# Kernel tuning notes

Hardware: AMD Instinct MI355X
Metric: run time of the kernel (lower is better)

The kernel has to match this reference:

```python
import jax, jax.numpy as jnp
import numpy as np
from jax.scipy.linalg import expm

B, S, D, E, K, NROT = 2, 2048, 1024, 8, 2, 3
EPS = 1e-5


def setup_inputs() -> dict:
    key = jax.random.key(0)
    ks = jax.random.split(key, 16)
    sc = 0.02
    x = jax.random.normal(ks[0], (B, S, D), jnp.float32)
    ln_gamma = 1.0 + sc * jax.random.normal(ks[1], (D,), jnp.float32)
    ln_beta = sc * jax.random.normal(ks[2], (D,), jnp.float32)
    abel_w = sc * jax.random.normal(ks[3], (D, D), jnp.float32)
    abel_b = sc * jax.random.normal(ks[4], (D,), jnp.float32)
    moe_gate_w = sc * jax.random.normal(ks[5], (D, E), jnp.float32)
    moe_gate_b = sc * jax.random.normal(ks[6], (E,), jnp.float32)
    ew1 = sc * jax.random.normal(ks[7], (E, D, 2 * D), jnp.float32)
    eb1 = sc * jax.random.normal(ks[8], (E, 2 * D), jnp.float32)
    ew2 = sc * jax.random.normal(ks[9], (E, 2 * D, D), jnp.float32)
    eb2 = sc * jax.random.normal(ks[10], (E, D), jnp.float32)
    g = sc * jax.random.normal(ks[11], (NROT, D, D), jnp.float32)
    gens = 0.5 * (g - jnp.swapaxes(g, -1, -2))  # skew-symmetric, as in reset_parameters
    gc_w = sc * jax.random.normal(ks[12], (2 * D, 1), jnp.float32)
    gc_b = sc * jax.random.normal(ks[13], (1,), jnp.float32)
    return dict(x=x, ln_gamma=ln_gamma, ln_beta=ln_beta, abel_w=abel_w, abel_b=abel_b,
                moe_gate_w=moe_gate_w, moe_gate_b=moe_gate_b, ew1=ew1, eb1=eb1,
                ew2=ew2, eb2=eb2, gens=gens, gc_w=gc_w, gc_b=gc_b)


def _gelu(x):
    return jax.nn.gelu(x, approximate=False)  # torch nn.GELU default = exact erf


def _forward(x, ln_gamma, ln_beta, abel_w, abel_b, moe_gate_w, moe_gate_b,
             ew1, eb1, ew2, eb2, gens, gc_w, gc_b):
    residual = x
    # LayerNorm
    mu = jnp.mean(x, axis=-1, keepdims=True)
    var = jnp.mean((x - mu) ** 2, axis=-1, keepdims=True)
    xn = (x - mu) * jax.lax.rsqrt(var + EPS) * ln_gamma + ln_beta
    # abel branch: Linear + GELU
    abel_out = _gelu(xn @ abel_w + abel_b)
    # MoE: dense all-experts compute, masked by top-k softmax weights
    logits = xn @ moe_gate_w + moe_gate_b                      # [B,S,E]
    topw, topi = jax.lax.top_k(logits, K)                      # [B,S,K]
    topw = jax.nn.softmax(topw, axis=-1)
    w_dense = jnp.sum(jax.nn.one_hot(topi, E, dtype=xn.dtype) * topw[..., None], axis=-2)  # [B,S,E]
    h = _gelu(jnp.einsum('bsd,edh->ebsh', xn, ew1) + eb1[:, None, None, :])  # [E,B,S,2D]
    eo = jnp.einsum('ebsh,ehd->ebsd', h, ew2) + eb2[:, None, None, :]        # [E,B,S,D]
    moe_out = jnp.einsum('ebsd,bse->bsd', eo, w_dense)
    # GeometricRotation: sequential matrix_exp rotations
    for i in range(NROT):
        moe_out = moe_out @ expm(gens[i])
    # gated residual mix
    combined = jnp.concatenate([abel_out, moe_out], axis=-1)
    gate = jax.nn.sigmoid(combined @ gc_w + gc_b)              # [B,S,1]
    mixed = abel_out * (1.0 - gate) + moe_out * gate
    return residual + mixed


def reference(x, ln_gamma, ln_beta, abel_w, abel_b, moe_gate_w, moe_gate_b,
              ew1, eb1, ew2, eb2, gens, gc_w, gc_b):
    return _forward(x, ln_gamma, ln_beta, abel_w, abel_b, moe_gate_w, moe_gate_b,
                    ew1, eb1, ew2, eb2, gens, gc_w, gc_b)
```

## Files before the change

kernel.cpp:

```cpp
#include <hip/hip_runtime.h>
#include <hip/hip_bf16.h>
#include <cstdint>
#include <cstddef>

#define DD   1024
#define DD2  2048
#define EE   8
#define NTOK 4096
#define CAPR 10240
#define MAXT1 72
#define MAXT2 40

typedef __bf16 bf16_t;
typedef __bf16 bf16x8 __attribute__((ext_vector_type(8)));
typedef __bf16 bf16x4 __attribute__((ext_vector_type(4)));
typedef float  f32x4v __attribute__((ext_vector_type(4)));

__device__ __forceinline__ float gelu_f(float v){
  const float t = v*(0.7978845608028654f + 0.0356774081f*v*v);
  const float u = __expf(2.0f*t);
  return __fdividef(v*u, 1.0f + u);
}

__device__ __forceinline__ void gload_lds16(const void* g, void* l){
  __builtin_amdgcn_global_load_lds(
    (const __attribute__((address_space(1))) unsigned int*)(uintptr_t)g,
    (__attribute__((address_space(3))) unsigned int*)(uintptr_t)l,
    16, 0, 0);
}

enum { EPI_GELU_F32=0, EPI_GELU_BF16=1, EPI_BIAS_BF16=2, EPI_SCALE_BF16=3,
       EPI_ADDV_BF16=4, EPI_BF16=5, EPI_F32=6 };

template<int BM,int BN,int WAVES,int EPI,bool TAB>
__global__ __launch_bounds__(WAVES*64)
void gemm_bt(const bf16_t* __restrict__ A, const bf16_t* __restrict__ Bt,
             const int N, const int K, const int gx, const int gy, const int gz,
             const long sAz, const long sBz, const long sOz,
             const int* __restrict__ tileE, const int* __restrict__ tileR,
             const int* __restrict__ ntp, const int* __restrict__ offp,
             const int* __restrict__ tokOf,
             const float* __restrict__ bias, const long sBias,
             const float alpha,
             const bf16_t* __restrict__ addv,
             float* __restrict__ outF, bf16_t* __restrict__ outB)
{
  constexpr int BK = 32;
  constexpr int WROWS = WAVES/2;
  constexpr int WM = BM/WROWS, WN = BN/2;
  constexpr int FM = WM/16, FN = WN/16;
  constexpr int IA = BM/(16*WAVES), IB = BN/(16*WAVES);
  constexpr int NLD = IA + IB;
  __shared__ alignas(16) bf16_t sA[3][BM*BK];
  __shared__ alignas(16) bf16_t sB[3][BN*BK];

  int bx, by, bz; long ro = 0;
  if constexpr (TAB) {
    const int nwg = gx * gy;
    const int q = nwg >> 3, r = nwg & 7;
    const int k = blockIdx.x & 7, i = blockIdx.x >> 3;
    if (i >= q + (k < r ? 1 : 0)) return;
    const int l = k * q + (k < r ? k : r) + i;
    const int ti = l / gx; bx = l - ti*gx;
    if (ti >= ntp[0]) return;
    bz = tileE[ti]; by = 0;
    ro = (long)offp[bz] + tileR[ti];
  } else {
    const int nwg = gx * gy * gz;
    const int q = nwg >> 3, r = nwg & 7;
    const int k = blockIdx.x & 7, i = blockIdx.x >> 3;
    if (i >= q + (k < r ? 1 : 0)) return;
    const int l = k * q + (k < r ? k : r) + i;
    bx = l % gx; const int t2 = l / gx; by = t2 % gy; bz = t2 / gy;
  }

  const int z = bz;
  const bf16_t* Bp = Bt + (size_t)z * sBz;
  float*  oF = outF;
  bf16_t* oB = outB;
  if constexpr (TAB) {
    oB += ro * (long)N;
  } else {
    A += (size_t)z * sAz;
    if (oF) oF += (size_t)z * sOz;
    if (oB) oB += (size_t)z * sOz;
  }
  const float*  bp = bias ? bias + (size_t)z * sBias : nullptr;
  const bf16_t* vp = addv ? addv + (size_t)z * sOz   : nullptr;

  const int tid = threadIdx.x;
  const int wid = tid >> 6, lid = tid & 63;
  const int wr = wid >> 1, wc = wid & 1;
  const int brow = by * BM, bcol = bx * BN;
  const int fr = lid & 15, fq = lid >> 4;
  const int rl = lid >> 2, qs = lid & 3;

  const char* aSrc[IA];
  const char* bSrc[IB];
  #pragma unroll
  for (int i = 0; i < IA; i++) {
    const int rloc = (wid*IA + i)*16 + rl;
    const int q = qs ^ ((rloc >> 1) & 3);
    const bf16_t* arow;
    if constexpr (TAB) {
      arow = tokOf ? (A + (size_t)tokOf[ro + rloc] * K)
                   : (A + (size_t)(ro + rloc) * K);
    } else {
      arow = A + (size_t)(brow + rloc) * K;
    }
    aSrc[i] = (const char*)arow + q*16;
  }
  #pragma unroll
  for (int i = 0; i < IB; i++) {
    const int rloc = (wid*IB + i)*16 + rl;
    const int q = qs ^ ((rloc >> 1) & 3);
    bSrc[i] = (const char*)(Bp + (size_t)(bcol + rloc) * K) + q*16;
  }

  f32x4v acc[FM][FN] = {};

  auto stage = [&](int buf, int kt) {
    #pragma unroll
    for (int i = 0; i < IA; i++)
      gload_lds16(aSrc[i] + (size_t)kt*2, (char*)sA[buf] + (wid*IA + i)*1024);
    #pragma unroll
    for (int i = 0; i < IB; i++)
      gload_lds16(bSrc[i] + (size_t)kt*2, (char*)sB[buf] + (wid*IB + i)*1024);
  };

  stage(0, 0);
  stage(1, BK);
  const int nk = K / BK;
  int b0 = 0, b1 = 1, b2 = 2;

  for (int t = 0; t < nk; ++t) {
    if (t < nk - 1) asm volatile("s_waitcnt vmcnt(%0)" :: "i"(NLD) : "memory");
    else            asm volatile("s_waitcnt vmcnt(0)" ::: "memory");
    __builtin_amdgcn_s_barrier();
    __builtin_amdgcn_sched_barrier(0);
    if (t + 2 < nk) stage(b2, (t + 2)*BK);

    bf16x8 af[FM], bb[FN];
    #pragma unroll
    for (int mi = 0; mi < FM; mi++) {
      const int r2 = wr*WM + mi*16 + fr;
      const int q = fq ^ ((r2 >> 1) & 3);
      af[mi] = *(const bf16x8*)((const char*)sA[b0] + r2*64 + q*16);
    }
    #pragma unroll
    for (int ni = 0; ni < FN; ni++) {
      const int r2 = wc*WN + ni*16 + fr;
      const int q = fq ^ ((r2 >> 1) & 3);
      bb[ni] = *(const bf16x8*)((const char*)sB[b0] + r2*64 + q*16);
    }
    #pragma unroll
    for (int mi = 0; mi < FM; mi++)
      #pragma unroll
      for (int ni = 0; ni < FN; ni++)
        acc[mi][ni] = __builtin_amdgcn_mfma_f32_16x16x32_bf16(
            af[mi], bb[ni], acc[mi][ni], 0, 0, 0);

    const int tb_ = b0; b0 = b1; b1 = b2; b2 = tb_;
  }

  #pragma unroll
  for (int mi = 0; mi < FM; mi++) {
    #pragma unroll
    for (int ni = 0; ni < FN; ni++) {
      const int rg0 = brow + wr*WM + mi*16 + fq*4;
      const int cg  = bcol + wc*WN + ni*16 + fr;
      #pragma unroll
      for (int i = 0; i < 4; i++) {
        const int rg = rg0 + i;
        float v = acc[mi][ni][i];
        if constexpr (EPI == EPI_GELU_F32) {
          v += bp[cg];
          oF[(size_t)rg*N + cg] = gelu_f(v);
        } else if constexpr (EPI == EPI_GELU_BF16) {
          v += bp[cg];
          oB[(size_t)rg*N + cg] = (bf16_t)gelu_f(v);
        } else if constexpr (EPI == EPI_BIAS_BF16) {
          v += bp[cg];
          oB[(size_t)rg*N + cg] = (bf16_t)v;
        } else if constexpr (EPI == EPI_SCALE_BF16) {
          oB[(size_t)rg*N + cg] = (bf16_t)(v * alpha);
        } else if constexpr (EPI == EPI_ADDV_BF16) {
          oB[(size_t)rg*N + cg] = (bf16_t)(v + (float)vp[(size_t)rg*N + cg]);
        } else if constexpr (EPI == EPI_BF16) {
          oB[(size_t)rg*N + cg] = (bf16_t)v;
        } else {
          oF[(size_t)rg*N + cg] = v;
        }
      }
    }
  }
}

struct TileRef { const float* src; bf16_t* dst; int R, C, bx, by; };

__device__ __forceinline__ TileRef resolve_tile(
    int ti, const float* abel_w, bf16_t* abel_wT,
    const float* ew1, bf16_t* ew1T, const float* ew2, bf16_t* ew2T){
  TileRef tr;
  if (ti < 256) {
    tr.src = abel_w; tr.dst = abel_wT; tr.R = DD; tr.C = DD;
    tr.bx = ti & 15; tr.by = ti >> 4;
  } else if (ti < 4352) {
    const int i = ti - 256, z = i >> 9, r = i & 511;
    tr.src = ew1 + (size_t)z*DD*DD2; tr.dst = ew1T + (size_t)z*DD2*DD;
    tr.R = DD; tr.C = DD2; tr.bx = r & 31; tr.by = r >> 5;
  } else {
    const int i = ti - 4352, z = i >> 9, r = i & 511;
    tr.src = ew2 + (size_t)z*DD2*DD; tr.dst = ew2T + (size_t)z*DD*DD2;
    tr.R = DD2; tr.C = DD; tr.bx = r & 15; tr.by = r >> 4;
  }
  return tr;
}

__global__ __launch_bounds__(256)
void prep_kernel(const float* __restrict__ abel_w, bf16_t* __restrict__ abel_wT,
                 const float* __restrict__ ew1, bf16_t* __restrict__ ew1T,
                 const float* __restrict__ ew2, bf16_t* __restrict__ ew2T,
                 const float* __restrict__ gens, bf16_t* __restrict__ Hn)
{
  const int bid = blockIdx.x;
  const int lx = threadIdx.x & 15, ly = threadIdx.x >> 4;
  if (bid < 4224) {
    __shared__ float t[64][65];
    const TileRef t0 = resolve_tile(bid*2,     abel_w, abel_wT, ew1, ew1T, ew2, ew2T);
    const TileRef t1 = resolve_tile(bid*2 + 1, abel_w, abel_wT, ew1, ew1T, ew2, ew2T);
    float4 g0[4], g1[4];
    #pragma unroll
    for (int i = 0; i < 4; i++)
      g0[i] = *(const float4*)(t0.src + (size_t)(t0.by*64 + ly + i*16)*t0.C + t0.bx*64 + lx*4);
    #pragma unroll
    for (int i = 0; i < 4; i++)
      g1[i] = *(const float4*)(t1.src + (size_t)(t1.by*64 + ly + i*16)*t1.C + t1.bx*64 + lx*4);
    #pragma unroll
    for (int i = 0; i < 4; i++) {
      t[ly + i*16][lx*4+0] = g0[i].x; t[ly + i*16][lx*4+1] = g0[i].y;
      t[ly + i*16][lx*4+2] = g0[i].z; t[ly + i*16][lx*4+3] = g0[i].w;
    }
    __syncthreads();
    #pragma unroll
    for (int i = 0; i < 4; i++) {
      const int c = t0.bx*64 + ly + i*16;
      bf16x4 o;
      #pragma unroll
      for (int j = 0; j < 4; j++) o[j] = (bf16_t)t[lx*4+j][ly + i*16];
      *(bf16x4*)(t0.dst + (size_t)c*t0.R + t0.by*64 + lx*4) = o;
    }
    __syncthreads();
    #pragma unroll
    for (int i = 0; i < 4; i++) {
      t[ly + i*16][lx*4+0] = g1[i].x; t[ly + i*16][lx*4+1] = g1[i].y;
      t[ly + i*16][lx*4+2] = g1[i].z; t[ly + i*16][lx*4+3] = g1[i].w;
    }
    __syncthreads();
    #pragma unroll
    for (int i = 0; i < 4; i++) {
      const int c = t1.bx*64 + ly + i*16;
      bf16x4 o;
      #pragma unroll
      for (int j = 0; j < 4; j++) o[j] = (bf16_t)t[lx*4+j][ly + i*16];
      *(bf16x4*)(t1.dst + (size_t)c*t1.R + t1.by*64 + lx*4) = o;
    }
  } else {
    #pragma unroll
    for (int it = 0; it < 4; it++) {
      const long i4 = (((long)(bid - 4224)*4 + it)*256 + threadIdx.x)*4;
      const float4 v = *(const float4*)(gens + i4);
      bf16x4 b; b[0]=(bf16_t)(-v.x); b[1]=(bf16_t)(-v.y);
      b[2]=(bf16_t)(-v.z); b[3]=(bf16_t)(-v.w);
      *(bf16x4*)(Hn + i4) = b;
    }
  }
}

__global__ __launch_bounds__(256)
void tb16_kernel(const bf16_t* __restrict__ Ut, bf16_t* __restrict__ Tb){
  __shared__ bf16_t tile[32][33];
  const bf16_t* src = Ut + (size_t)(1 - blockIdx.z) * DD * DD;
  bf16_t*       dst = Tb + (size_t)blockIdx.z * DD * DD;
  const int c0 = blockIdx.x*32, r0 = blockIdx.y*32;
  #pragma unroll
  for (int i = 0; i < 4; i++)
    tile[threadIdx.y + i*8][threadIdx.x] = src[(size_t)(r0 + threadIdx.y + i*8)*DD + c0 + threadIdx.x];
  __syncthreads();
  #pragma unroll
  for (int i = 0; i < 4; i++)
    dst[(size_t)(c0 + threadIdx.y + i*8)*DD + r0 + threadIdx.x] = tile[threadIdx.x][threadIdx.y + i*8];
}

__global__ __launch_bounds__(256)
void vw_kernel(const bf16_t* __restrict__ Hn, const bf16_t* __restrict__ H2,
               bf16_t* __restrict__ Vb, bf16_t* __restrict__ Wtb){
  const long i0 = ((long)blockIdx.x*256 + threadIdx.x)*4;
  const long rc = i0 % (long)(DD*DD);
  const int r = (int)(rc / DD), c0 = (int)(rc % DD);
  const bf16x4 h  = *(const bf16x4*)(Hn + i0);
  const bf16x4 h2 = *(const bf16x4*)(H2 + i0);
  bf16x4 v, w;
  #pragma unroll
  for (int j = 0; j < 4; j++) {
    const float d  = (r == c0 + j) ? 1.0f : 0.0f;
    const float fh = (float)h[j], f2 = (float)h2[j];
    v[j] = (bf16_t)(d + fh + f2*0.5f);
    w[j] = (bf16_t)(d*(1.0f/6.0f) - fh*(1.0f/24.0f) + f2*(1.0f/120.0f));
  }
  *(bf16x4*)(Vb  + i0) = v;
  *(bf16x4*)(Wtb + i0) = w;
}

__global__ __launch_bounds__(256)
void ln_gate_kernel(const float* __restrict__ x, const float* __restrict__ gamma,
                    const float* __restrict__ beta, const float* __restrict__ gw,
                    const float* __restrict__ gb,
                    bf16_t* __restrict__ xnb, int2* __restrict__ ids,
                    float2* __restrict__ wts)
{
  const int t = blockIdx.x, tid = threadIdx.x, j0 = tid*4;
  const int wid = tid >> 6, lid = tid & 63;
  const float4 v = *(const float4*)(x + (size_t)t*DD + j0);
  float s  = v.x + v.y + v.z + v.w;
  float ss = v.x*v.x + v.y*v.y + v.z*v.z + v.w*v.w;
  #pragma unroll
  for (int off = 32; off; off >>= 1) { s += __shfl_down(s, off); ss += __shfl_down(ss, off); }
  __shared__ float redS[4], redQ[4], mv[2];
  if (lid == 0) { redS[wid] = s; redQ[wid] = ss; }
  __syncthreads();
  if (tid == 0) {
    const float S1 = redS[0]+redS[1]+redS[2]+redS[3];
    const float S2 = redQ[0]+redQ[1]+redQ[2]+redQ[3];
    const float mu  = S1 * (1.0f/DD);
    const float var = S2 * (1.0f/DD) - mu*mu;
    mv[0] = mu; mv[1] = rsqrtf(var + 1e-5f);
  }
  __syncthreads();
  const float mu = mv[0], rstd = mv[1];
  const float4 g = *(const float4*)(gamma + j0);
  const float4 b = *(const float4*)(beta  + j0);
  float xn[4];
  xn[0] = (v.x-mu)*rstd*g.x + b.x;
  xn[1] = (v.y-mu)*rstd*g.y + b.y;
  xn[2] = (v.z-mu)*rstd*g.z + b.z;
  xn[3] = (v.w-mu)*rstd*g.w + b.w;
  bf16x4 ov; ov[0]=(bf16_t)xn[0]; ov[1]=(bf16_t)xn[1]; ov[2]=(bf16_t)xn[2]; ov[3]=(bf16_t)xn[3];
  *(bf16x4*)(xnb + (size_t)t*DD + j0) = ov;

  float p[8] = {0,0,0,0,0,0,0,0};
  #pragma unroll
  for (int i = 0; i < 4; i++) {
    const float4 a0 = *(const float4*)(gw + (size_t)(j0+i)*EE);
    const float4 a1 = *(const float4*)(gw + (size_t)(j0+i)*EE + 4);
    const float xv = xn[i];
    p[0]+=xv*a0.x; p[1]+=xv*a0.y; p[2]+=xv*a0.z; p[3]+=xv*a0.w;
    p[4]+=xv*a1.x; p[5]+=xv*a1.y; p[6]+=xv*a1.z; p[7]+=xv*a1.w;
  }
  #pragma unroll
  for (int off = 32; off; off >>= 1) {
    #pragma unroll
    for (int e = 0; e < 8; e++) p[e] += __shfl_down(p[e], off);
  }
  __shared__ float pr[32];
  if (lid == 0) {
    #pragma unroll
    for (int e = 0; e < 8; e++) pr[wid*8 + e] = p[e];
  }
  __syncthreads();
  if (tid == 0) {
    float l[8];
    #pragma unroll
    for (int e = 0; e < 8; e++) l[e] = pr[e] + pr[8+e] + pr[16+e] + pr[24+e] + gb[e];
    int i1 = 0; float m1 = l[0];
    #pragma unroll
    for (int e = 1; e < 8; e++) if (l[e] > m1) { m1 = l[e]; i1 = e; }
    int i2 = 0; float m2 = -1e30f;
    #pragma unroll
    for (int e = 0; e < 8; e++) if (e != i1 && l[e] > m2) { m2 = l[e]; i2 = e; }
    const float wa = 1.0f/(1.0f + expf(m2 - m1));
    ids[t] = make_int2(i1, i2);
    wts[t] = make_float2(wa, 1.0f - wa);
  }
}

__global__ __launch_bounds__(256)
void route_kernel(const int2* __restrict__ ids, int* __restrict__ slotA,
                  int* __restrict__ slotB, int* __restrict__ cnt,
                  int* __restrict__ off, int* __restrict__ tE1,
                  int* __restrict__ tR1, int* __restrict__ tE2,
                  int* __restrict__ tR2, int* __restrict__ ntp)
{
  const int tid = threadIdx.x;
  const int wid = tid >> 6, lid = tid & 63;
  __shared__ int wsum[EE][4];
  __shared__ int base[EE];
  if (tid < EE) base[tid] = 0;
  __syncthreads();
  const unsigned long long lt = (1ull << lid) - 1ull;
  for (int c0 = 0; c0 < NTOK; c0 += 256) {
    const int t = c0 + tid;
    const int2 id = ids[t];
    int pA = 0, pB = 0;
    #pragma unroll
    for (int e = 0; e < EE; e++) {
      const bool fA = (id.x == e), fB = (id.y == e);
      const unsigned long long mA = __ballot(fA);
      const unsigned long long mB = __ballot(fB);
      const int cA = __popcll(mA);
      if (lid == 0) wsum[e][wid] = cA + __popcll(mB);
      if (fA) pA = __popcll(mA & lt);
      if (fB) pB = cA + __popcll(mB & lt);
    }
    __syncthreads();
    int wbA = base[id.x], wbB = base[id.y];
    for (int w = 0; w < wid; w++) { wbA += wsum[id.x][w]; wbB += wsum[id.y][w]; }
    slotA[t] = wbA + pA;
    slotB[t] = wbB + pB;
    __syncthreads();
    if (tid < EE) base[tid] += wsum[tid][0]+wsum[tid][1]+wsum[tid][2]+wsum[tid][3];
    __syncthreads();
  }
  if (tid == 0) {
    int a = 0, n1 = 0, n2 = 0;
    for (int e = 0; e < EE; e++) {
      cnt[e] = base[e]; off[e] = a;
      for (int r2 = 0; r2 < base[e]; r2 += 128) { tE1[n1] = e; tR1[n1] = r2; n1++; }
      for (int r2 = 0; r2 < base[e]; r2 += 256) { tE2[n2] = e; tR2[n2] = r2; n2++; }
      a += (base[e] + 255) & ~255;
    }
    ntp[0] = n1; ntp[1] = n2;
  }
}

__global__ __launch_bounds__(256)
void fill_tok_kernel(const int2* __restrict__ ids, const int* __restrict__ slotA,
                     const int* __restrict__ slotB, const int* __restrict__ off,
                     const int* __restrict__ cnt, int* __restrict__ tokOf){
  const int t = blockIdx.x*256 + threadIdx.x;
  const int2 id = ids[t];
  tokOf[off[id.x] + slotA[t]] = t;
  tokOf[off[id.y] + slotB[t]] = t;
  if (blockIdx.x == 0) {
    for (int e = 0; e < EE; e++) {
      const int c = cnt[e], o = off[e], al = (c + 255) & ~255;
      for (int p = c + threadIdx.x; p < al; p += 256) tokOf[o + p] = 0;
    }
  }
}

__global__ __launch_bounds__(256)
void combine_kernel(const bf16_t* __restrict__ Yg, const int2* __restrict__ ids,
                    const int* __restrict__ slotA, const int* __restrict__ slotB,
                    const int* __restrict__ off, const float2* __restrict__ wts,
                    bf16_t* __restrict__ Xa){
  const int t = blockIdx.x, j = threadIdx.x*4;
  const int2 id = ids[t];
  const float2 w = wts[t];
  const bf16x4 a = *(const bf16x4*)(Yg + (size_t)(off[id.x] + slotA[t])*DD + j);
  const bf16x4 b = *(const bf16x4*)(Yg + (size_t)(off[id.y] + slotB[t])*DD + j);
  bf16x4 o;
  #pragma unroll
  for (int i = 0; i < 4; i++) o[i] = (bf16_t)(w.x*(float)a[i] + w.y*(float)b[i]);
  *(bf16x4*)(Xa + (size_t)t*DD + j) = o;
}

__global__ __launch_bounds__(256)
void mix_kernel(const float* __restrict__ x, const bf16_t* __restrict__ abel,
                const float* __restrict__ rot, const float* __restrict__ gcw,
                const float* __restrict__ gcb, float* __restrict__ out)
{
  const int t = blockIdx.x, tid = threadIdx.x, j0 = tid*4;
  const int wid = tid >> 6, lid = tid & 63;
  const bf16x4 ab = *(const bf16x4*)(abel + (size_t)t*DD + j0);
  const float4 r  = *(const float4*)(rot  + (size_t)t*DD + j0);
  const float4 ga = *(const float4*)(gcw + j0);
  const float4 gr = *(const float4*)(gcw + DD + j0);
  const float a0 = (float)ab[0], a1 = (float)ab[1], a2 = (float)ab[2], a3 = (float)ab[3];
  float p = a0*ga.x + a1*ga.y + a2*ga.z + a3*ga.w
          + r.x*gr.x + r.y*gr.y + r.z*gr.z + r.w*gr.w;
  #pragma unroll
  for (int off = 32; off; off >>= 1) p += __shfl_down(p, off);
  __shared__ float red[4];
  __shared__ float gsh;
  if (lid == 0) red[wid] = p;
  __syncthreads();
  if (tid == 0) {
    const float P = red[0] + red[1] + red[2] + red[3] + gcb[0];
    gsh = 1.0f/(1.0f + expf(-P));
  }
  __syncthreads();
  const float gate = gsh, g1 = 1.0f - gate;
  const float4 xv = *(const float4*)(x + (size_t)t*DD + j0);
  float4 o;
  o.x = xv.x + a0*g1 + r.x*gate;
  o.y = xv.y + a1*g1 + r.y*gate;
  o.z = xv.z + a2*g1 + r.z*gate;
  o.w = xv.w + a3*g1 + r.w*gate;
  *(float4*)(out + (size_t)t*DD + j0) = o;
}

extern "C" void kernel_launch(void* const* d_in, const int* in_sizes, int n_in,
                              void* d_out, int out_size, void* d_ws, size_t ws_size,
                              hipStream_t stream)
{
  (void)in_sizes; (void)n_in; (void)out_size; (void)ws_size;
  const float* x      = (const float*)d_in[0];
  const float* ln_g   = (const float*)d_in[1];
  const float* ln_b   = (const float*)d_in[2];
  const float* abel_w = (const float*)d_in[3];
  const float* abel_b = (const float*)d_in[4];
  const float* gate_w = (const float*)d_in[5];
  const float* gate_b = (const float*)d_in[6];
  const float* ew1    = (const float*)d_in[7];
  const float* eb1    = (const float*)d_in[8];
  const float* ew2    = (const float*)d_in[9];
  const float* eb2    = (const float*)d_in[10];
  const float* gens   = (const float*)d_in[11];
  const float* gc_w   = (const float*)d_in[12];
  const float* gc_b   = (const float*)d_in[13];
  float* out = (float*)d_out;

  char* wsp = (char*)d_ws;
  auto alloc = [&](size_t bytes) -> char* {
    char* p = wsp; wsp += (bytes + 255) & ~(size_t)255; return p;
  };
  const size_t MB = 1u<<20;
  bf16_t* xnb   = (bf16_t*)alloc((size_t)NTOK*DD*2);
  int2*   ids   = (int2*)  alloc((size_t)NTOK*8);
  float2* wts   = (float2*)alloc((size_t)NTOK*8);
  int*    slotA = (int*)   alloc((size_t)NTOK*4);
  int*    slotB = (int*)   alloc((size_t)NTOK*4);
  int*    cnt   = (int*)   alloc(64);
  int*    off   = (int*)   alloc(64);
  int*    tE1   = (int*)   alloc(MAXT1*4);
  int*    tR1   = (int*)   alloc(MAXT1*4);
  int*    tE2   = (int*)   alloc(MAXT2*4);
  int*    tR2   = (int*)   alloc(MAXT2*4);
  int*    ntp   = (int*)   alloc(64);
  int*    tokOf = (int*)   alloc((size_t)CAPR*4);
  bf16_t* abel_wT = (bf16_t*)alloc((size_t)DD*DD*2);
  char*   UN      = alloc(64*MB);
  bf16_t* ew1T  = (bf16_t*)UN;
  bf16_t* ew2T  = (bf16_t*)(UN + 32*MB);
  bf16_t* Hn    = (bf16_t*)alloc((size_t)3*DD*DD*2);
  bf16_t* abelo = (bf16_t*)alloc((size_t)NTOK*DD*2);
  bf16_t* Yg    = (bf16_t*)alloc((size_t)CAPR*DD*2);
  bf16_t* Hg    = (bf16_t*)alloc((size_t)CAPR*DD2*2);
  bf16_t* Xa    = (bf16_t*)alloc((size_t)NTOK*DD*2);
  float*  rot   = (float*)Hg;
  bf16_t* H2  = (bf16_t*)(UN + 0*MB);
  bf16_t* H3  = (bf16_t*)(UN + 6*MB);
  bf16_t* Vb  = (bf16_t*)(UN + 12*MB);
  bf16_t* Wtb = (bf16_t*)(UN + 18*MB);
  bf16_t* Ut  = (bf16_t*)(UN + 24*MB);
  bf16_t* Tb  = (bf16_t*)(UN + 30*MB);
  bf16_t* Pb  = (bf16_t*)(UN + 34*MB);
  bf16_t* Rt  = (bf16_t*)(UN + 36*MB);
  const long D2 = (long)DD*DD;

  auto gflat = [](int gx, int gy, int gz) {
    const int nwg = gx*gy*gz; return 8 * ((nwg + 7) / 8);
  };

  prep_kernel<<<dim3(4992,1,1), 256, 0, stream>>>(abel_w, abel_wT, ew1, ew1T,
                                                  ew2, ew2T, gens, Hn);

  ln_gate_kernel<<<dim3(NTOK,1,1), 256, 0, stream>>>(x, ln_g, ln_b, gate_w, gate_b,
                                                     xnb, ids, wts);
  route_kernel<<<dim3(1,1,1), 256, 0, stream>>>(ids, slotA, slotB, cnt, off,
                                                tE1, tR1, tE2, tR2, ntp);
  fill_tok_kernel<<<dim3(NTOK/256,1,1), 256, 0, stream>>>(ids, slotA, slotB, off, cnt, tokOf);

  gemm_bt<256,128,8,EPI_GELU_BF16,true><<<dim3(gflat(DD2/128, MAXT2, 1),1,1), 512, 0, stream>>>(
      xnb, ew1T, DD2, DD, DD2/128, MAXT2, 1, 0, (long)DD2*DD, 0,
      tE2, tR2, ntp + 1, off, tokOf, eb1, DD2, 1.0f, nullptr, nullptr, Hg);
  gemm_bt<128,128,4,EPI_BIAS_BF16,true><<<dim3(gflat(DD/128, MAXT1, 1),1,1), 256, 0, stream>>>(
      Hg, ew2T, DD, DD2, DD/128, MAXT1, 1, 0, (long)DD*DD2, 0,
      tE1, tR1, ntp, off, nullptr, eb2, DD, 1.0f, nullptr, nullptr, Yg);
  combine_kernel<<<dim3(NTOK,1,1), 256, 0, stream>>>(Yg, ids, slotA, slotB, off, wts, Xa);

  gemm_bt<128,128,4,EPI_GELU_BF16,false><<<dim3(gflat(8,32,1),1,1), 256, 0, stream>>>(
      xnb, abel_wT, DD, DD, 8, 32, 1, 0, 0, 0, nullptr, nullptr, nullptr, nullptr,
      nullptr, abel_b, 0, 1.0f, nullptr, nullptr, abelo);

  gemm_bt<64,64,4,EPI_SCALE_BF16,false><<<dim3(gflat(16,16,3),1,1), 256, 0, stream>>>(
      Hn, Hn, DD, DD, 16, 16, 3, D2, D2, D2, nullptr, nullptr, nullptr, nullptr,
      nullptr, nullptr, 0, -1.0f, nullptr, nullptr, H2);
  gemm_bt<64,64,4,EPI_SCALE_BF16,false><<<dim3(gflat(16,16,3),1,1), 256, 0, stream>>>(
      H2, Hn, DD, DD, 16, 16, 3, D2, D2, D2, nullptr, nullptr, nullptr, nullptr,
      nullptr, nullptr, 0, -1.0f, nullptr, nullptr, H3);
  vw_kernel<<<dim3(3*DD*DD/1024,1,1), 256, 0, stream>>>(Hn, H2, Vb, Wtb);
  gemm_bt<64,64,4,EPI_ADDV_BF16,false><<<dim3(gflat(16,16,3),1,1), 256, 0, stream>>>(
      H3, Wtb, DD, DD, 16, 16, 3, D2, D2, D2, nullptr, nullptr, nullptr, nullptr,
      nullptr, nullptr, 0, 1.0f, Vb, nullptr, Ut);
  tb16_kernel<<<dim3(32,32,2), dim3(32,8,1), 0, stream>>>(Ut, Tb);
  gemm_bt<64,64,4,EPI_BF16,false><<<dim3(gflat(16,16,1),1,1), 256, 0, stream>>>(
      Ut + 2*D2, Tb, DD, DD, 16, 16, 1, 0, 0, 0, nullptr, nullptr, nullptr, nullptr,
      nullptr, nullptr, 0, 1.0f, nullptr, nullptr, Pb);
  gemm_bt<64,64,4,EPI_BF16,false><<<dim3(gflat(16,16,1),1,1), 256, 0, stream>>>(
      Pb, Tb + D2, DD, DD, 16, 16, 1, 0, 0, 0, nullptr, nullptr, nullptr, nullptr,
      nullptr, nullptr, 0, 1.0f, nullptr, nullptr, Rt);
  gemm_bt<128,128,4,EPI_F32,false><<<dim3(gflat(8,32,1),1,1), 256, 0, stream>>>(
      Xa, Rt, DD, DD, 8, 32, 1, 0, 0, 0, nullptr, nullptr, nullptr, nullptr,
      nullptr, nullptr, 0, 1.0f, nullptr, rot, nullptr);

  mix_kernel<<<dim3(NTOK,1,1), 256, 0, stream>>>(x, abelo, rot, gc_w, gc_b, out);
}
```

Before: 337.8 us.

## Fuse abel GEMM into expert-1 grouped GEMM and merge LN/gate with weight prep

```diff
diff --git a/kernel.cpp b/kernel.cpp
--- a/kernel.cpp
+++ b/kernel.cpp
@@ -9,7 +9,7 @@
 #define NTOK 4096
 #define CAPR 10240
 #define MAXT1 72
-#define MAXT2 40
+#define MAXT2 56
 
 typedef __bf16 bf16_t;
 typedef __bf16 bf16x8 __attribute__((ext_vector_type(8)));
@@ -43,6 +43,8 @@
              const float* __restrict__ bias, const long sBias,
              const float alpha,
              const bf16_t* __restrict__ addv,
+             const bf16_t* __restrict__ abelB, const float* __restrict__ abelBias,
+             bf16_t* __restrict__ abelOut, const int aN, const int aGx,
              float* __restrict__ outF, bf16_t* __restrict__ outB)
 {
   constexpr int BK = 32;
@@ -64,7 +66,8 @@
     const int ti = l / gx; bx = l - ti*gx;
     if (ti >= ntp[0]) return;
     bz = tileE[ti]; by = 0;
-    ro = (long)offp[bz] + tileR[ti];
+    if (bz == EE) { if (bx >= aGx) return; ro = tileR[ti]; }
+    else          { ro = (long)offp[bz] + tileR[ti]; }
   } else {
     const int nwg = gx * gy * gz;
     const int q = nwg >> 3, r = nwg & 7;
@@ -75,23 +78,33 @@
   }
 
   const int z = bz;
-  const bf16_t* Bp = Bt + (size_t)z * sBz;
+  const bool abelT = TAB && (z == EE);
+  int NN = abelT ? aN : N;
+  const bool useTok = TAB && !abelT && (tokOf != nullptr);
+  const bf16_t* Bp;
+  const float*  bp;
   float*  oF = outF;
-  bf16_t* oB = outB;
-  if constexpr (TAB) {
-    oB += ro * (long)N;
+  bf16_t* oB;
+  if (abelT) {
+    Bp = abelB; bp = abelBias;
+    oB = abelOut + ro * (long)aN;
+  } else if constexpr (TAB) {
+    Bp = Bt + (size_t)z * sBz;
+    bp = bias ? bias + (size_t)z * sBias : nullptr;
+    oB = outB + ro * (long)N;
   } else {
+    Bp = Bt + (size_t)z * sBz;
+    bp = bias ? bias + (size_t)z * sBias : nullptr;
     A += (size_t)z * sAz;
+    oB = outB; if (oB) oB += (size_t)z * sOz;
     if (oF) oF += (size_t)z * sOz;
-    if (oB) oB += (size_t)z * sOz;
-  }
-  const float*  bp = bias ? bias + (size_t)z * sBias : nullptr;
-  const bf16_t* vp = addv ? addv + (size_t)z * sOz   : nullptr;
+  }
+  const bf16_t* vp = addv ? addv + (size_t)z * sOz : nullptr;
 
   const int tid = threadIdx.x;
   const int wid = tid >> 6, lid = tid & 63;
   const int wr = wid >> 1, wc = wid & 1;
-  const int brow = by * BM, bcol = bx * BN;
+  const int brow = (TAB ? 0 : by * BM), bcol = bx * BN;
   const int fr = lid & 15, fq = lid >> 4;
   const int rl = lid >> 2, qs = lid & 3;
 
@@ -103,8 +116,8 @@
     const int q = qs ^ ((rloc >> 1) & 3);
     const bf16_t* arow;
     if constexpr (TAB) {
-      arow = tokOf ? (A + (size_t)tokOf[ro + rloc] * K)
-                   : (A + (size_t)(ro + rloc) * K);
+      arow = useTok ? (A + (size_t)tokOf[ro + rloc] * K)
+                    : (A + (size_t)(ro + rloc) * K);
     } else {
       arow = A + (size_t)(brow + rloc) * K;
     }
@@ -175,42 +188,42 @@
         float v = acc[mi][ni][i];
         if constexpr (EPI == EPI_GELU_F32) {
           v += bp[cg];
-          oF[(size_t)rg*N + cg] = gelu_f(v);
+          oF[(size_t)rg*NN + cg] = gelu_f(v);
         } else if constexpr (EPI == EPI_GELU_BF16) {
           v += bp[cg];
-          oB[(size_t)rg*N + cg] = (bf16_t)gelu_f(v);
+          oB[(size_t)rg*NN + cg] = (bf16_t)gelu_f(v);
         } else if constexpr (EPI == EPI_BIAS_BF16) {
           v += bp[cg];
-          oB[(size_t)rg*N + cg] = (bf16_t)v;
+          oB[(size_t)rg*NN + cg] = (bf16_t)v;
         } else if constexpr (EPI == EPI_SCALE_BF16) {
-          oB[(size_t)rg*N + cg] = (bf16_t)(v * alpha);
+          oB[(size_t)rg*NN + cg] = (bf16_t)(v * alpha);
         } else if constexpr (EPI == EPI_ADDV_BF16) {
-          oB[(size_t)rg*N + cg] = (bf16_t)(v + (float)vp[(size_t)rg*N + cg]);
+          oB[(size_t)rg*NN + cg] = (bf16_t)(v + (float)vp[(size_t)rg*NN + cg]);
         } else if constexpr (EPI == EPI_BF16) {
-          oB[(size_t)rg*N + cg] = (bf16_t)v;
+          oB[(size_t)rg*NN + cg] = (bf16_t)v;
         } else {
-          oF[(size_t)rg*N + cg] = v;
+          oF[(size_t)rg*NN + cg] = v;
         }
       }
     }
   }
 }
 
-struct TileRef { const float* src; bf16_t* dst; int R, C, bx, by; };
-
-__device__ __forceinline__ TileRef resolve_tile(
+struct TRef { const float* src; bf16_t* dst; int R, C, bx, by; };
+
+__device__ __forceinline__ TRef resolve256(
     int ti, const float* abel_w, bf16_t* abel_wT,
     const float* ew1, bf16_t* ew1T, const float* ew2, bf16_t* ew2T){
-  TileRef tr;
-  if (ti < 256) {
+  TRef tr;
+  if (ti < 64) {
     tr.src = abel_w; tr.dst = abel_wT; tr.R = DD; tr.C = DD;
     tr.bx = ti & 15; tr.by = ti >> 4;
-  } else if (ti < 4352) {
-    const int i = ti - 256, z = i >> 9, r = i & 511;
+  } else if (ti < 1088) {
+    const int i = ti - 64, z = i >> 7, r = i & 127;
     tr.src = ew1 + (size_t)z*DD*DD2; tr.dst = ew1T + (size_t)z*DD2*DD;
     tr.R = DD; tr.C = DD2; tr.bx = r & 31; tr.by = r >> 5;
   } else {
-    const int i = ti - 4352, z = i >> 9, r = i & 511;
+    const int i = ti - 1088, z = i >> 7, r = i & 127;
     tr.src = ew2 + (size_t)z*DD2*DD; tr.dst = ew2T + (size_t)z*DD*DD2;
     tr.R = DD2; tr.C = DD; tr.bx = r & 15; tr.by = r >> 4;
   }
@@ -218,57 +231,107 @@
 }
 
 __global__ __launch_bounds__(256)
-void prep_kernel(const float* __restrict__ abel_w, bf16_t* __restrict__ abel_wT,
-                 const float* __restrict__ ew1, bf16_t* __restrict__ ew1T,
-                 const float* __restrict__ ew2, bf16_t* __restrict__ ew2T,
-                 const float* __restrict__ gens, bf16_t* __restrict__ Hn)
+void pre_kernel(const float* __restrict__ x, const float* __restrict__ gamma,
+                const float* __restrict__ beta, const float* __restrict__ gw,
+                const float* __restrict__ gb,
+                bf16_t* __restrict__ xnb, int2* __restrict__ ids,
+                float2* __restrict__ wts,
+                const float* __restrict__ abel_w, bf16_t* __restrict__ abel_wT,
+                const float* __restrict__ ew1, bf16_t* __restrict__ ew1T,
+                const float* __restrict__ ew2, bf16_t* __restrict__ ew2T,
+                const float* __restrict__ gens, bf16_t* __restrict__ Hn)
 {
-  const int bid = blockIdx.x;
-  const int lx = threadIdx.x & 15, ly = threadIdx.x >> 4;
-  if (bid < 4224) {
-    __shared__ float t[64][65];
-    const TileRef t0 = resolve_tile(bid*2,     abel_w, abel_wT, ew1, ew1T, ew2, ew2T);
-    const TileRef t1 = resolve_tile(bid*2 + 1, abel_w, abel_wT, ew1, ew1T, ew2, ew2T);
-    float4 g0[4], g1[4];
-    #pragma unroll
-    for (int i = 0; i < 4; i++)
-      g0[i] = *(const float4*)(t0.src + (size_t)(t0.by*64 + ly + i*16)*t0.C + t0.bx*64 + lx*4);
-    #pragma unroll
-    for (int i = 0; i < 4; i++)
-      g1[i] = *(const float4*)(t1.src + (size_t)(t1.by*64 + ly + i*16)*t1.C + t1.bx*64 + lx*4);
+  __shared__ bf16_t tb[64][260];
+  __shared__ float redS[4], redQ[4], mv[2], pr[32];
+  const int bid = blockIdx.x, tid = threadIdx.x;
+
+  if (bid < 4096) {
+    const int t = bid, j0 = tid*4;
+    const int wid = tid >> 6, lid = tid & 63;
+    const float4 v = *(const float4*)(x + (size_t)t*DD + j0);
+    float s  = v.x + v.y + v.z + v.w;
+    float ss = v.x*v.x + v.y*v.y + v.z*v.z + v.w*v.w;
+    #pragma unroll
+    for (int off = 32; off; off >>= 1) { s += __shfl_down(s, off); ss += __shfl_down(ss, off); }
+    if (lid == 0) { redS[wid] = s; redQ[wid] = ss; }
+    __syncthreads();
+    if (tid == 0) {
+      const float S1 = redS[0]+redS[1]+redS[2]+redS[3];
+      const float S2 = redQ[0]+redQ[1]+redQ[2]+redQ[3];
+      const float mu  = S1 * (1.0f/DD);
+      const float var = S2 * (1.0f/DD) - mu*mu;
+      mv[0] = mu; mv[1] = rsqrtf(var + 1e-5f);
+    }
+    __syncthreads();
+    const float mu = mv[0], rstd = mv[1];
+    const float4 g = *(const float4*)(gamma + j0);
+    const float4 b = *(const float4*)(beta  + j0);
+    float xn[4];
+    xn[0] = (v.x-mu)*rstd*g.x + b.x;
+    xn[1] = (v.y-mu)*rstd*g.y + b.y;
+    xn[2] = (v.z-mu)*rstd*g.z + b.z;
+    xn[3] = (v.w-mu)*rstd*g.w + b.w;
+    bf16x4 ov; ov[0]=(bf16_t)xn[0]; ov[1]=(bf16_t)xn[1]; ov[2]=(bf16_t)xn[2]; ov[3]=(bf16_t)xn[3];
+    *(bf16x4*)(xnb + (size_t)t*DD + j0) = ov;
+
+    float p[8] = {0,0,0,0,0,0,0,0};
     #pragma unroll
     for (int i = 0; i < 4; i++) {
-      t[ly + i*16][lx*4+0] = g0[i].x; t[ly + i*16][lx*4+1] = g0[i].y;
-      t[ly + i*16][lx*4+2] = g0[i].z; t[ly + i*16][lx*4+3] = g0[i].w;
+      const float4 a0 = *(const float4*)(gw + (size_t)(j0+i)*EE);
+      const float4 a1 = *(const float4*)(gw + (size_t)(j0+i)*EE + 4);
+      const float xv = xn[i];
+      p[0]+=xv*a0.x; p[1]+=xv*a0.y; p[2]+=xv*a0.z; p[3]+=xv*a0.w;
+      p[4]+=xv*a1.x; p[5]+=xv*a1.y; p[6]+=xv*a1.z; p[7]+=xv*a1.w;
+    }
+    #pragma unroll
+    for (int off = 32; off; off >>= 1) {
+      #pragma unroll
+      for (int e = 0; e < 8; e++) p[e] += __shfl_down(p[e], off);
+    }
+    if (lid == 0) {
+      #pragma unroll
+      for (int e = 0; e < 8; e++) pr[wid*8 + e] = p[e];
     }
     __syncthreads();
-    #pragma unroll
-    for (int i = 0; i < 4; i++) {
-      const int c = t0.bx*64 + ly + i*16;
-      bf16x4 o;
+    if (tid == 0) {
+      float l[8];
       #pragma unroll
-      for (int j = 0; j < 4; j++) o[j] = (bf16_t)t[lx*4+j][ly + i*16];
-      *(bf16x4*)(t0.dst + (size_t)c*t0.R + t0.by*64 + lx*4) = o;
+      for (int e = 0; e < 8; e++) l[e] = pr[e] + pr[8+e] + pr[16+e] + pr[24+e] + gb[e];
+      int i1 = 0; float m1 = l[0];
+      #pragma unroll
+      for (int e = 1; e < 8; e++) if (l[e] > m1) { m1 = l[e]; i1 = e; }
+      int i2 = 0; float m2 = -1e30f;
+      #pragma unroll
+      for (int e = 0; e < 8; e++) if (e != i1 && l[e] > m2) { m2 = l[e]; i2 = e; }
+      const float wa = 1.0f/(1.0f + expf(m2 - m1));
+      ids[t] = make_int2(i1, i2);
+      wts[t] = make_float2(wa, 1.0f - wa);
+    }
+  } else if (bid < 6208) {
+    const TRef tr = resolve256(bid - 4096, abel_w, abel_wT, ew1, ew1T, ew2, ew2T);
+    const int lx = tid & 15, ly = tid >> 4;
+    const int r0 = tr.by*256, c0 = tr.bx*64;
+    #pragma unroll
+    for (int i = 0; i < 16; i++) {
+      const int r = ly + i*16;
+      const float4 v = *(const float4*)(tr.src + (size_t)(r0 + r)*tr.C + c0 + lx*4);
+      tb[lx*4+0][r] = (bf16_t)v.x;
+      tb[lx*4+1][r] = (bf16_t)v.y;
+      tb[lx*4+2][r] = (bf16_t)v.z;
+      tb[lx*4+3][r] = (bf16_t)v.w;
     }
     __syncthreads();
-    #pragma unroll
-    for (int i = 0; i < 4; i++) {
-      t[ly + i*16][lx*4+0] = g1[i].x; t[ly + i*16][lx*4+1] = g1[i].y;
-      t[ly + i*16][lx*4+2] = g1[i].z; t[ly + i*16][lx*4+3] = g1[i].w;
-    }
-    __syncthreads();
-    #pragma unroll
-    for (int i = 0; i < 4; i++) {
-      const int c = t1.bx*64 + ly + i*16;
-      bf16x4 o;
-      #pragma unroll
-      for (int j = 0; j < 4; j++) o[j] = (bf16_t)t[lx*4+j][ly + i*16];
-      *(bf16x4*)(t1.dst + (size_t)c*t1.R + t1.by*64 + lx*4) = o;
+    const int w = tid >> 6, l = tid & 63;
+    #pragma unroll
+    for (int i = 0; i < 16; i++) {
+      const int c = w*16 + i;
+      const bf16x4 o = *(const bf16x4*)(&tb[c][l*4]);
+      *(bf16x4*)(tr.dst + (size_t)(c0 + c)*tr.R + r0 + l*4) = o;
     }
   } else {
     #pragma unroll
     for (int it = 0; it < 4; it++) {
-      const long i4 = (((long)(bid - 4224)*4 + it)*256 + threadIdx.x)*4;
+      const long i4 = (((long)(bid - 6208)*4 + it)*256 + tid)*4;
       const float4 v = *(const float4*)(gens + i4);
       bf16x4 b; b[0]=(bf16_t)(-v.x); b[1]=(bf16_t)(-v.y);
       b[2]=(bf16_t)(-v.z); b[3]=(bf16_t)(-v.w);
@@ -310,78 +373,6 @@
   }
   *(bf16x4*)(Vb  + i0) = v;
   *(bf16x4*)(Wtb + i0) = w;
-}
-
-__global__ __launch_bounds__(256)
-void ln_gate_kernel(const float* __restrict__ x, const float* __restrict__ gamma,
-                    const float* __restrict__ beta, const float* __restrict__ gw,
-                    const float* __restrict__ gb,
-                    bf16_t* __restrict__ xnb, int2* __restrict__ ids,
-                    float2* __restrict__ wts)
-{
-  const int t = blockIdx.x, tid = threadIdx.x, j0 = tid*4;
-  const int wid = tid >> 6, lid = tid & 63;
-  const float4 v = *(const float4*)(x + (size_t)t*DD + j0);
-  float s  = v.x + v.y + v.z + v.w;
-  float ss = v.x*v.x + v.y*v.y + v.z*v.z + v.w*v.w;
-  #pragma unroll
-  for (int off = 32; off; off >>= 1) { s += __shfl_down(s, off); ss += __shfl_down(ss, off); }
-  __shared__ float redS[4], redQ[4], mv[2];
-  if (lid == 0) { redS[wid] = s; redQ[wid] = ss; }
-  __syncthreads();
-  if (tid == 0) {
-    const float S1 = redS[0]+redS[1]+redS[2]+redS[3];
-    const float S2 = redQ[0]+redQ[1]+redQ[2]+redQ[3];
-    const float mu  = S1 * (1.0f/DD);
-    const float var = S2 * (1.0f/DD) - mu*mu;
-    mv[0] = mu; mv[1] = rsqrtf(var + 1e-5f);
-  }
-  __syncthreads();
-  const float mu = mv[0], rstd = mv[1];
-  const float4 g = *(const float4*)(gamma + j0);
-  const float4 b = *(const float4*)(beta  + j0);
-  float xn[4];
-  xn[0] = (v.x-mu)*rstd*g.x + b.x;
-  xn[1] = (v.y-mu)*rstd*g.y + b.y;
-  xn[2] = (v.z-mu)*rstd*g.z + b.z;
-  xn[3] = (v.w-mu)*rstd*g.w + b.w;
-  bf16x4 ov; ov[0]=(bf16_t)xn[0]; ov[1]=(bf16_t)xn[1]; ov[2]=(bf16_t)xn[2]; ov[3]=(bf16_t)xn[3];
-  *(bf16x4*)(xnb + (size_t)t*DD + j0) = ov;
-
-  float p[8] = {0,0,0,0,0,0,0,0};
-  #pragma unroll
-  for (int i = 0; i < 4; i++) {
-    const float4 a0 = *(const float4*)(gw + (size_t)(j0+i)*EE);
-    const float4 a1 = *(const float4*)(gw + (size_t)(j0+i)*EE + 4);
-    const float xv = xn[i];
-    p[0]+=xv*a0.x; p[1]+=xv*a0.y; p[2]+=xv*a0.z; p[3]+=xv*a0.w;
-    p[4]+=xv*a1.x; p[5]+=xv*a1.y; p[6]+=xv*a1.z; p[7]+=xv*a1.w;
-  }
-  #pragma unroll
-  for (int off = 32; off; off >>= 1) {
-    #pragma unroll
-    for (int e = 0; e < 8; e++) p[e] += __shfl_down(p[e], off);
-  }
-  __shared__ float pr[32];
-  if (lid == 0) {
-    #pragma unroll
-    for (int e = 0; e < 8; e++) pr[wid*8 + e] = p[e];
-  }
-  __syncthreads();
-  if (tid == 0) {
-    float l[8];
-    #pragma unroll
-    for (int e = 0; e < 8; e++) l[e] = pr[e] + pr[8+e] + pr[16+e] + pr[24+e] + gb[e];
-    int i1 = 0; float m1 = l[0];
-    #pragma unroll
-    for (int e = 1; e < 8; e++) if (l[e] > m1) { m1 = l[e]; i1 = e; }
-    int i2 = 0; float m2 = -1e30f;
-    #pragma unroll
-    for (int e = 0; e < 8; e++) if (e != i1 && l[e] > m2) { m2 = l[e]; i2 = e; }
-    const float wa = 1.0f/(1.0f + expf(m2 - m1));
-    ids[t] = make_int2(i1, i2);
-    wts[t] = make_float2(wa, 1.0f - wa);
-  }
 }
 
 __global__ __launch_bounds__(256)
@@ -429,6 +420,7 @@
       for (int r2 = 0; r2 < base[e]; r2 += 256) { tE2[n2] = e; tR2[n2] = r2; n2++; }
       a += (base[e] + 255) & ~255;
     }
+    for (int m = 0; m < NTOK/256; m++) { tE2[n2] = EE; tR2[n2] = m*256; n2++; }
     ntp[0] = n1; ntp[1] = n2;
   }
 }
@@ -563,47 +555,50 @@
     const int nwg = gx*gy*gz; return 8 * ((nwg + 7) / 8);
   };
 
-  prep_kernel<<<dim3(4992,1,1), 256, 0, stream>>>(abel_w, abel_wT, ew1, ew1T,
-                                                  ew2, ew2T, gens, Hn);
-
-  ln_gate_kernel<<<dim3(NTOK,1,1), 256, 0, stream>>>(x, ln_g, ln_b, gate_w, gate_b,
-                                                     xnb, ids, wts);
+  pre_kernel<<<dim3(6976,1,1), 256, 0, stream>>>(
+      x, ln_g, ln_b, gate_w, gate_b, xnb, ids, wts,
+      abel_w, abel_wT, ew1, ew1T, ew2, ew2T, gens, Hn);
+
   route_kernel<<<dim3(1,1,1), 256, 0, stream>>>(ids, slotA, slotB, cnt, off,
                                                 tE1, tR1, tE2, tR2, ntp);
   fill_tok_kernel<<<dim3(NTOK/256,1,1), 256, 0, stream>>>(ids, slotA, slotB, off, cnt, tokOf);
 
   gemm_bt<256,128,8,EPI_GELU_BF16,true><<<dim3(gflat(DD2/128, MAXT2, 1),1,1), 512, 0, stream>>>(
       xnb, ew1T, DD2, DD, DD2/128, MAXT2, 1, 0, (long)DD2*DD, 0,
-      tE2, tR2, ntp + 1, off, tokOf, eb1, DD2, 1.0f, nullptr, nullptr, Hg);
+      tE2, tR2, ntp + 1, off, tokOf, eb1, DD2, 1.0f, nullptr,
+      abel_wT, abel_b, abelo, DD, DD/128, nullptr, Hg);
   gemm_bt<128,128,4,EPI_BIAS_BF16,true><<<dim3(gflat(DD/128, MAXT1, 1),1,1), 256, 0, stream>>>(
       Hg, ew2T, DD, DD2, DD/128, MAXT1, 1, 0, (long)DD*DD2, 0,
-      tE1, tR1, ntp, off, nullptr, eb2, DD, 1.0f, nullptr, nullptr, Yg);
+      tE1, tR1, ntp, off, nullptr, eb2, DD, 1.0f, nullptr,
+      nullptr, nullptr, nullptr, 0, 0, nullptr, Yg);
   combine_kernel<<<dim3(NTOK,1,1), 256, 0, stream>>>(Yg, ids, slotA, slotB, off, wts, Xa);
-
-  gemm_bt<128,128,4,EPI_GELU_BF16,false><<<dim3(gflat(8,32,1),1,1), 256, 0, stream>>>(
-      xnb, abel_wT, DD, DD, 8, 32, 1, 0, 0, 0, nullptr, nullptr, nullptr, nullptr,
-      nullptr, abel_b, 0, 1.0f, nullptr, nullptr, abelo);
 
   gemm_bt<64,64,4,EPI_SCALE_BF16,false><<<dim3(gflat(16,16,3),1,1), 256, 0, stream>>>(
       Hn, Hn, DD, DD, 16, 16, 3, D2, D2, D2, nullptr, nullptr, nullptr, nullptr,
-      nullptr, nullptr, 0, -1.0f, nullptr, nullptr, H2);
+      nullptr, nullptr, 0, -1.0f, nullptr,
+      nullptr, nullptr, nullptr, 0, 0, nullptr, H2);
   gemm_bt<64,64,4,EPI_SCALE_BF16,false><<<dim3(gflat(16,16,3),1,1), 256, 0, stream>>>(
       H2, Hn, DD, DD, 16, 16, 3, D2, D2, D2, nullptr, nullptr, nullptr, nullptr,
-      nullptr, nullptr, 0, -1.0f, nullptr, nullptr, H3);
+      nullptr, nullptr, 0, -1.0f, nullptr,
+      nullptr, nullptr, nullptr, 0, 0, nullptr, H3);
   vw_kernel<<<dim3(3*DD*DD/1024,1,1), 256, 0, stream>>>(Hn, H2, Vb, Wtb);
   gemm_bt<64,64,4,EPI_ADDV_BF16,false><<<dim3(gflat(16,16,3),1,1), 256, 0, stream>>>(
       H3, Wtb, DD, DD, 16, 16, 3, D2, D2, D2, nullptr, nullptr, nullptr, nullptr,
-      nullptr, nullptr, 0, 1.0f, Vb, nullptr, Ut);
+      nullptr, nullptr, 0, 1.0f, Vb,
+      nullptr, nullptr, nullptr, 0, 0, nullptr, Ut);
   tb16_kernel<<<dim3(32,32,2), dim3(32,8,1), 0, stream>>>(Ut, Tb);
   gemm_bt<64,64,4,EPI_BF16,false><<<dim3(gflat(16,16,1),1,1), 256, 0, stream>>>(
       Ut + 2*D2, Tb, DD, DD, 16, 16, 1, 0, 0, 0, nullptr, nullptr, nullptr, nullptr,
-      nullptr, nullptr, 0, 1.0f, nullptr, nullptr, Pb);
+      nullptr, nullptr, 0, 1.0f, nullptr,
+      nullptr, nullptr, nullptr, 0, 0, nullptr, Pb);
   gemm_bt<64,64,4,EPI_BF16,false><<<dim3(gflat(16,16,1),1,1), 256, 0, stream>>>(
       Pb, Tb + D2, DD, DD, 16, 16, 1, 0, 0, 0, nullptr, nullptr, nullptr, nullptr,
-      nullptr, nullptr, 0, 1.0f, nullptr, nullptr, Rt);
+      nullptr, nullptr, 0, 1.0f, nullptr,
+      nullptr, nullptr, nullptr, 0, 0, nullptr, Rt);
   gemm_bt<128,128,4,EPI_F32,false><<<dim3(gflat(8,32,1),1,1), 256, 0, stream>>>(
       Xa, Rt, DD, DD, 8, 32, 1, 0, 0, 0, nullptr, nullptr, nullptr, nullptr,
-      nullptr, nullptr, 0, 1.0f, nullptr, rot, nullptr);
+      nullptr, nullptr, 0, 1.0f, nullptr,
+      nullptr, nullptr, nullptr, 0, 0, rot, nullptr);
 
   mix_kernel<<<dim3(NTOK,1,1), 256, 0, stream>>>(x, abelo, rot, gc_w, gc_b, out);
 }
```

Measured after the change: 341.1 us. Within noise of the previous version (+1.0%).
